# Kernel optimization log

Measured on AMD Instinct MI355X. Metric: run time of the kernel, lower is better.

The kernel has to match this reference:

```python
import jax, jax.numpy as jnp
import numpy as np

NUM_LEVELS = 16
LEVEL_DIM = 2
BASE_RES = 16
PER_LEVEL_SCALE = 2.0
LOG2_HASHMAP = 19
INPUT_DIM = 3
N_POINTS = 2_000_000
B = 262144


def _compute_offsets():
    offsets = []
    off = 0
    max_params = 2 ** LOG2_HASHMAP
    for i in range(NUM_LEVELS):
        res = int(np.ceil(BASE_RES * PER_LEVEL_SCALE ** i))
        p = min(max_params, (res + 1) ** INPUT_DIM)  # align_corners=False -> res+1 verts per axis
        p = int(np.ceil(p / 8) * 8)
        offsets.append(off)
        off += p
    offsets.append(off)
    return offsets

OFFSETS = _compute_offsets()
TOTAL_PARAMS = OFFSETS[-1]  # 7131240
PRIMES = (1, 2654435761, 805459861)  # instant-ngp fast_hash primes for D=3
CORNER_BITS = np.array([[(c >> d) & 1 for d in range(3)] for c in range(8)], dtype=np.int32)  # [8,3]


def _build_table(embeddings, fs_embeddings, scatter_index):
    # scatter_add point embeddings (and counts) into grid vertices, then blend
    sums = jnp.zeros((TOTAL_PARAMS, LEVEL_DIM), embeddings.dtype).at[scatter_index].add(embeddings)
    counts = jnp.zeros((TOTAL_PARAMS,), embeddings.dtype).at[scatter_index].add(1.0)
    sel = jnp.minimum(counts, 1.0)[:, None]
    num = jnp.maximum(counts, 1.0)[:, None]
    return (sums / num) * sel + fs_embeddings * (1.0 - sel)


def _grid_encode(x, table):
    # x: [B,3] in [0,1]; table: [TOTAL_PARAMS, C]. Multi-res hash grid, linear interp,
    # align_corners=False (matches torch-ngp grid_encode CUDA kernel).
    S = np.log2(PER_LEVEL_SCALE)
    bits_i = jnp.asarray(CORNER_BITS)                 # [8,3] int
    bits_f = jnp.asarray(CORNER_BITS, dtype=x.dtype)  # [8,3] float
    outs = []
    for level in range(NUM_LEVELS):
        scale = np.exp2(level * S) * BASE_RES - 1.0
        resolution = int(np.ceil(scale)) + 1
        hashmap_size = OFFSETS[level + 1] - OFFSETS[level]
        pos = x * scale + 0.5  # align_corners=False offset
        pos_grid = jnp.floor(pos)
        frac = pos - pos_grid                                  # [B,3]
        corner = pos_grid.astype(jnp.int32)[:, None, :] + bits_i  # [B,8,3]
        stride = (resolution + 1) ** 3
        if stride > hashmap_size:
            # hashed level: xor of per-dim prime products, uint32 wraparound
            cu = corner.astype(jnp.uint32)
            idx = (cu[..., 0] * jnp.uint32(PRIMES[0])) ^ \
                  (cu[..., 1] * jnp.uint32(PRIMES[1])) ^ \
                  (cu[..., 2] * jnp.uint32(PRIMES[2]))
            idx = (idx % jnp.uint32(hashmap_size)).astype(jnp.int32)
        else:
            # dense level: row-major index with stride (res+1)
            r1 = resolution + 1
            idx = (corner[..., 0] + corner[..., 1] * r1 + corner[..., 2] * (r1 * r1)) % hashmap_size
        vals = table[idx + OFFSETS[level]]  # [B,8,C] gather
        w = jnp.prod(jnp.where(bits_f > 0, frac[:, None, :], 1.0 - frac[:, None, :]), axis=-1)  # [B,8]
        outs.append(jnp.einsum('bk,bkc->bc', w, vals))
    return jnp.concatenate(outs, axis=-1)  # [B, L*C]


def setup_inputs() -> dict:
    key = jax.random.key(0)
    k1, k2, k3, k4 = jax.random.split(key, 4)
    std = 1e-4  # reset_parameters() uniform(-1e-4, 1e-4)
    inputs = jax.random.uniform(k1, (B, 3), jnp.float32, minval=-1.0, maxval=1.0)
    embeddings = jax.random.uniform(k2, (N_POINTS, LEVEL_DIM), jnp.float32, minval=-std, maxval=std)
    fs_embeddings = jax.random.uniform(k3, (TOTAL_PARAMS, LEVEL_DIM), jnp.float32, minval=-std, maxval=std)
    scatter_index = jax.random.randint(k4, (N_POINTS,), 0, TOTAL_PARAMS, dtype=jnp.int32)
    return {"inputs": inputs, "embeddings": embeddings, "fs_embeddings": fs_embeddings,
            "scatter_index": scatter_index, "bound": 1}


def reference(inputs, embeddings, fs_embeddings, scatter_index, bound):
    table = _build_table(embeddings, fs_embeddings, scatter_index)
    x = (inputs + bound) / (2.0 * bound)  # map to [0,1]
    return _grid_encode(x, table)  # [B, NUM_LEVELS*LEVEL_DIM]
```

## Files before the change

### kernel.cpp

```cpp
#include <hip/hip_runtime.h>

#define TOTAL_PARAMS 7131240
#define NLEVELS 16
#define NB 262144
#define HASH_MASK 0x7FFFF

#define SF2 5115000.0f
#define CF 1e-4f

__constant__ int c_off[NLEVELS] = {
    0, 4920, 40864, 315496, 839784, 1364072, 1888360, 2412648,
    2936936, 3461224, 3985512, 4509800, 5034088, 5558376, 6082664, 6606952};

typedef float vfloat2 __attribute__((ext_vector_type(2)));
typedef float vfloat4 __attribute__((ext_vector_type(4)));
typedef unsigned vuint2 __attribute__((ext_vector_type(2)));
typedef int vint2 __attribute__((ext_vector_type(2)));

__global__ __launch_bounds__(256) void scatter_prep_kernel(
    const vfloat4* __restrict__ emb2, const vint2* __restrict__ sidx2,
    unsigned* __restrict__ accum, int n, int nsb,
    const float* __restrict__ x, const int* __restrict__ bound_p,
    vfloat4* __restrict__ xn, int B) {
    if ((int)blockIdx.x >= nsb) {
        int p = ((int)blockIdx.x - nsb) * 256 + threadIdx.x;
        if (p >= B) return;
        float bound = (float)bound_p[0];
        float denom = 2.0f * bound;
        vfloat4 o;
        o.x = (x[p * 3 + 0] + bound) / denom;
        o.y = (x[p * 3 + 1] + bound) / denom;
        o.z = (x[p * 3 + 2] + bound) / denom;
        o.w = 0.0f;
        xn[p] = o;
        return;
    }
    int i = blockIdx.x * 256 + threadIdx.x;
    int base = i * 2;
    if (base >= n) return;
    if (base + 1 < n) {
        vint2 idx = __builtin_nontemporal_load(&sidx2[i]);
        vfloat4 e = __builtin_nontemporal_load(&emb2[i]);
        unsigned qx0 = __float2uint_rn((e.x + CF) * SF2);
        unsigned qy0 = __float2uint_rn((e.y + CF) * SF2);
        unsigned qx1 = __float2uint_rn((e.z + CF) * SF2);
        unsigned qy1 = __float2uint_rn((e.w + CF) * SF2);
        atomicAdd(&accum[idx.x], (1u << 28) | (qx0 << 14) | qy0);
        atomicAdd(&accum[idx.y], (1u << 28) | (qx1 << 14) | qy1);
    } else {
        const int* sidx = (const int*)sidx2;
        const vfloat2* emb = (const vfloat2*)emb2;
        int idx = sidx[base];
        vfloat2 e = emb[base];
        unsigned qx = __float2uint_rn((e.x + CF) * SF2);
        unsigned qy = __float2uint_rn((e.y + CF) * SF2);
        atomicAdd(&accum[idx], (1u << 28) | (qx << 14) | qy);
    }
}

__device__ __forceinline__ unsigned short f2bf(float f) {
    unsigned u = __builtin_bit_cast(unsigned, f);
    return (unsigned short)((u + 0x7FFFu + ((u >> 16) & 1u)) >> 16);
}

__global__ __launch_bounds__(256) void finalize_kernel(
    const unsigned* __restrict__ accum, const vfloat4* __restrict__ fs2,
    unsigned long long* __restrict__ table2, int npairs) {
    int i = blockIdx.x * 256 + threadIdx.x;
    if (i >= npairs) return;
    vuint2 a = __builtin_nontemporal_load((const vuint2*)(accum + 2 * i));
    unsigned c0 = a.x >> 28, c1 = a.y >> 28;
    vfloat4 f = {0.0f, 0.0f, 0.0f, 0.0f};
    if ((c0 == 0u) | (c1 == 0u)) f = __builtin_nontemporal_load(&fs2[i]);
    float rx0, ry0, rx1, ry1;
    if (c0 == 0u) {
        rx0 = f.x; ry0 = f.y;
    } else {
        float inv = 1.0f / ((float)c0 * SF2);
        rx0 = (float)((a.x >> 14) & 0x3FFFu) * inv - CF;
        ry0 = (float)(a.x & 0x3FFFu) * inv - CF;
    }
    if (c1 == 0u) {
        rx1 = f.z; ry1 = f.w;
    } else {
        float inv = 1.0f / ((float)c1 * SF2);
        rx1 = (float)((a.y >> 14) & 0x3FFFu) * inv - CF;
        ry1 = (float)(a.y & 0x3FFFu) * inv - CF;
    }
    unsigned lo = (unsigned)f2bf(rx0) | ((unsigned)f2bf(ry0) << 16);
    unsigned hi = (unsigned)f2bf(rx1) | ((unsigned)f2bf(ry1) << 16);
    table2[i] = (unsigned long long)lo | ((unsigned long long)hi << 32);
}

template <bool DENSE>
__device__ __forceinline__ vfloat2 level_interp(
    float px, float py, float pz, int l, const unsigned* __restrict__ table_bf) {
    int res = 16 << l;
    float scale = (float)(res - 1);
    float posx = px * scale + 0.5f;
    float posy = py * scale + 0.5f;
    float posz = pz * scale + 0.5f;
    float gx = floorf(posx), gy = floorf(posy), gz = floorf(posz);
    float fx = posx - gx, fy = posy - gy, fz = posz - gz;
    unsigned ix = (unsigned)(int)gx, iy = (unsigned)(int)gy, iz = (unsigned)(int)gz;

    const unsigned* __restrict__ tb = table_bf + c_off[l];

    unsigned tyz[4];
    if (DENSE) {
        unsigned r1u = (unsigned)(res + 1);
        unsigned r1sq = r1u * r1u;
        unsigned ty0 = iy * r1u, tz0 = iz * r1sq;
        tyz[0] = ty0 + tz0;
        tyz[1] = ty0 + r1u + tz0;
        tyz[2] = ty0 + tz0 + r1sq;
        tyz[3] = ty0 + r1u + tz0 + r1sq;
    } else {
        unsigned ty0 = iy * 2654435761u, ty1 = ty0 + 2654435761u;
        unsigned tz0 = iz * 805459861u, tz1 = tz0 + 805459861u;
        tyz[0] = ty0 ^ tz0;
        tyz[1] = ty1 ^ tz0;
        tyz[2] = ty0 ^ tz1;
        tyz[3] = ty1 ^ tz1;
    }

    unsigned v[8];
#pragma unroll
    for (int c = 0; c < 8; ++c) {
        unsigned cx = ix + (unsigned)(c & 1);
        unsigned idx;
        if (DENSE) idx = cx + tyz[c >> 1];
        else       idx = (cx ^ tyz[c >> 1]) & HASH_MASK;
        v[c] = tb[idx];
    }

    float wy0 = 1.0f - fy, wz0 = 1.0f - fz;
    float wyz[4] = {wy0 * wz0, fy * wz0, wy0 * fz, fy * fz};
    float wx0 = 1.0f - fx;
    float ax = 0.0f, ay = 0.0f;
#pragma unroll
    for (int c2 = 0; c2 < 4; ++c2) {
        float v0x = __builtin_bit_cast(float, v[2 * c2] << 16);
        float v0y = __builtin_bit_cast(float, v[2 * c2] & 0xFFFF0000u);
        float v1x = __builtin_bit_cast(float, v[2 * c2 + 1] << 16);
        float v1y = __builtin_bit_cast(float, v[2 * c2 + 1] & 0xFFFF0000u);
        float w = wyz[c2];
        ax += w * (wx0 * v0x + fx * v1x);
        ay += w * (wx0 * v0y + fx * v1y);
    }
    vfloat2 r;
    r.x = ax;
    r.y = ay;
    return r;
}

struct v2x2 { vfloat2 a, b; };

__device__ __forceinline__ void hash_idx8(
    float px, float py, float pz, float scale,
    unsigned idx[8], float* fx, float* fy, float* fz) {
    float posx = px * scale + 0.5f;
    float posy = py * scale + 0.5f;
    float posz = pz * scale + 0.5f;
    float gx = floorf(posx), gy = floorf(posy), gz = floorf(posz);
    *fx = posx - gx; *fy = posy - gy; *fz = posz - gz;
    unsigned ix = (unsigned)(int)gx, iy = (unsigned)(int)gy, iz = (unsigned)(int)gz;
    unsigned ty0 = iy * 2654435761u, ty1 = ty0 + 2654435761u;
    unsigned tz0 = iz * 805459861u, tz1 = tz0 + 805459861u;
    unsigned tyz[4] = {ty0 ^ tz0, ty1 ^ tz0, ty0 ^ tz1, ty1 ^ tz1};
#pragma unroll
    for (int c = 0; c < 8; ++c)
        idx[c] = ((ix + (unsigned)(c & 1)) ^ tyz[c >> 1]) & HASH_MASK;
}

__device__ __forceinline__ vfloat2 wsum8(
    const unsigned v[8], float fx, float fy, float fz) {
    float wy0 = 1.0f - fy, wz0 = 1.0f - fz;
    float wyz[4] = {wy0 * wz0, fy * wz0, wy0 * fz, fy * fz};
    float wx0 = 1.0f - fx;
    float ax = 0.0f, ay = 0.0f;
#pragma unroll
    for (int c2 = 0; c2 < 4; ++c2) {
        float v0x = __builtin_bit_cast(float, v[2 * c2] << 16);
        float v0y = __builtin_bit_cast(float, v[2 * c2] & 0xFFFF0000u);
        float v1x = __builtin_bit_cast(float, v[2 * c2 + 1] << 16);
        float v1y = __builtin_bit_cast(float, v[2 * c2 + 1] & 0xFFFF0000u);
        float w = wyz[c2];
        ax += w * (wx0 * v0x + fx * v1x);
        ay += w * (wx0 * v0y + fx * v1y);
    }
    vfloat2 r;
    r.x = ax;
    r.y = ay;
    return r;
}

__global__ __launch_bounds__(256, 6) void encode_hash_kernel(
    const vfloat4* __restrict__ xn, const unsigned* __restrict__ table_bf,
    vfloat2* __restrict__ lm) {
    int l = 15 - ((int)blockIdx.x >> 9);
    int b0 = (((int)blockIdx.x & 511) << 9) + (int)threadIdx.x;
    int b1 = b0 + 256;

    vfloat4 pA = xn[b0];
    vfloat4 pB = xn[b1];

    int res = 16 << l;
    float scale = (float)(res - 1);
    const unsigned* __restrict__ tb = table_bf + c_off[l];

    unsigned iA[8], iB[8];
    float fAx, fAy, fAz, fBx, fBy, fBz;
    hash_idx8(pA.x, pA.y, pA.z, scale, iA, &fAx, &fAy, &fAz);
    hash_idx8(pB.x, pB.y, pB.z, scale, iB, &fBx, &fBy, &fBz);

    unsigned vA[8], vB[8];
#pragma unroll
    for (int c = 0; c < 8; ++c) vA[c] = tb[iA[c]];
#pragma unroll
    for (int c = 0; c < 8; ++c) vB[c] = tb[iB[c]];

    vfloat2 oA = wsum8(vA, fAx, fAy, fAz);
    vfloat2 oB = wsum8(vB, fBx, fBy, fBz);

    vfloat2* dst = &lm[(l - 3) * NB];
    __builtin_nontemporal_store(oA, dst + b0);
    __builtin_nontemporal_store(oB, dst + b1);
}

__global__ __launch_bounds__(256, 4) void finish_kernel(
    const vfloat4* __restrict__ xn, const unsigned* __restrict__ table_bf,
    const vfloat2* __restrict__ lm, float* __restrict__ out) {
    int b = blockIdx.x * 256 + threadIdx.x;

    vfloat4 p = xn[b];

    float row[2 * NLEVELS];

#pragma unroll
    for (int lev = 0; lev < 13; ++lev) {
        vfloat2 v = lm[lev * NB + b];
        row[2 * (lev + 3)] = v.x;
        row[2 * (lev + 3) + 1] = v.y;
    }
#pragma unroll
    for (int l = 0; l < 3; ++l) {
        vfloat2 o = level_interp<true>(p.x, p.y, p.z, l, table_bf);
        row[2 * l] = o.x;
        row[2 * l + 1] = o.y;
    }

    vfloat4* op = (vfloat4*)&out[b * 32];
#pragma unroll
    for (int k = 0; k < 8; ++k) {
        vfloat4 o;
        o.x = row[4 * k + 0];
        o.y = row[4 * k + 1];
        o.z = row[4 * k + 2];
        o.w = row[4 * k + 3];
        op[k] = o;
    }
}

extern "C" void kernel_launch(void* const* d_in, const int* in_sizes, int n_in,
                              void* d_out, int out_size, void* d_ws, size_t ws_size,
                              hipStream_t stream) {
    const float* x     = (const float*)d_in[0];
    const float* emb   = (const float*)d_in[1];
    const float* fs    = (const float*)d_in[2];
    const int*   sidx  = (const int*)d_in[3];
    const int*   bound = (const int*)d_in[4];

    unsigned* accum    = (unsigned*)d_ws;
    unsigned* table_bf = accum + TOTAL_PARAMS;
    vfloat4*  xn       = (vfloat4*)(table_bf + TOTAL_PARAMS);
    vfloat2*  lm       = (vfloat2*)d_ws;

    int npts = in_sizes[3];
    int B = in_sizes[0] / 3;

    (void)hipMemsetAsync(d_ws, 0, (size_t)TOTAL_PARAMS * sizeof(unsigned), stream);

    int npair_pts = (npts + 1) / 2;
    int nsb = (npair_pts + 255) / 256;
    int npb = (B + 255) / 256;
    scatter_prep_kernel<<<nsb + npb, 256, 0, stream>>>(
        (const vfloat4*)emb, (const vint2*)sidx, accum, npts, nsb,
        x, bound, xn, B);

    int npairs = TOTAL_PARAMS / 2;
    finalize_kernel<<<(npairs + 255) / 256, 256, 0, stream>>>(
        accum, (const vfloat4*)fs, (unsigned long long*)table_bf, npairs);

    encode_hash_kernel<<<13 * (B / 512), 256, 0, stream>>>(
        xn, table_bf, lm);

    finish_kernel<<<B / 256, 256, 0, stream>>>(
        xn, table_bf, lm, (float*)d_out);
}
```

Baseline: 319.3 us.

## Replace global atomic scatter with bucketed binning and shared-memory accumulation

The global-memory atomicAdd scatter over a 28MB accumulator is replaced by a two-pass scheme. Points are first binned into 871 buckets of 8192 slots, with one global atomic per point on a bucket counter and the record written to a per-bucket array. A per-bucket kernel then accumulates the records with LDS atomics and builds the bf16 table directly, which removes the large accumulator memset and the separate finalize pass. In exchange each point adds an 8-byte record write and read, heavy contention on the bucket counters, and records past the fixed capacity of 4032 per bucket are silently dropped.

```diff
diff --git a/kernel.cpp b/kernel.cpp
--- a/kernel.cpp
+++ b/kernel.cpp
@@ -8,6 +8,11 @@
 #define SF2 5115000.0f
 #define CF 1e-4f
 
+#define BKT_SH 13
+#define BKT_SLOTS 8192
+#define NBKT 871
+#define BKT_CAP 4032
+
 __constant__ int c_off[NLEVELS] = {
     0, 4920, 40864, 315496, 839784, 1364072, 1888360, 2412648,
     2936936, 3461224, 3985512, 4509800, 5034088, 5558376, 6082664, 6606952};
@@ -15,15 +20,17 @@
 typedef float vfloat2 __attribute__((ext_vector_type(2)));
 typedef float vfloat4 __attribute__((ext_vector_type(4)));
 typedef unsigned vuint2 __attribute__((ext_vector_type(2)));
-typedef int vint2 __attribute__((ext_vector_type(2)));
-
-__global__ __launch_bounds__(256) void scatter_prep_kernel(
-    const vfloat4* __restrict__ emb2, const vint2* __restrict__ sidx2,
-    unsigned* __restrict__ accum, int n, int nsb,
+typedef unsigned vuint4 __attribute__((ext_vector_type(4)));
+typedef int vint4 __attribute__((ext_vector_type(4)));
+
+__global__ __launch_bounds__(256) void binscatter_prep_kernel(
+    const float* __restrict__ emb, const int* __restrict__ sidx,
+    unsigned long long* __restrict__ rec, unsigned* __restrict__ cnt,
+    int n, int nab,
     const float* __restrict__ x, const int* __restrict__ bound_p,
     vfloat4* __restrict__ xn, int B) {
-    if ((int)blockIdx.x >= nsb) {
-        int p = ((int)blockIdx.x - nsb) * 256 + threadIdx.x;
+    if ((int)blockIdx.x >= nab) {
+        int p = ((int)blockIdx.x - nab) * 256 + threadIdx.x;
         if (p >= B) return;
         float bound = (float)bound_p[0];
         float denom = 2.0f * bound;
@@ -35,26 +42,44 @@
         xn[p] = o;
         return;
     }
-    int i = blockIdx.x * 256 + threadIdx.x;
-    int base = i * 2;
-    if (base >= n) return;
-    if (base + 1 < n) {
-        vint2 idx = __builtin_nontemporal_load(&sidx2[i]);
-        vfloat4 e = __builtin_nontemporal_load(&emb2[i]);
-        unsigned qx0 = __float2uint_rn((e.x + CF) * SF2);
-        unsigned qy0 = __float2uint_rn((e.y + CF) * SF2);
-        unsigned qx1 = __float2uint_rn((e.z + CF) * SF2);
-        unsigned qy1 = __float2uint_rn((e.w + CF) * SF2);
-        atomicAdd(&accum[idx.x], (1u << 28) | (qx0 << 14) | qy0);
-        atomicAdd(&accum[idx.y], (1u << 28) | (qx1 << 14) | qy1);
+    int i0 = ((int)blockIdx.x * 256 + (int)threadIdx.x) * 8;
+    if (i0 >= n) return;
+    if (i0 + 8 <= n) {
+        vint4 s0 = __builtin_nontemporal_load((const vint4*)(sidx + i0));
+        vint4 s1 = __builtin_nontemporal_load((const vint4*)(sidx + i0 + 4));
+        vfloat4 e0 = __builtin_nontemporal_load((const vfloat4*)(emb + 2 * i0));
+        vfloat4 e1 = __builtin_nontemporal_load((const vfloat4*)(emb + 2 * i0 + 4));
+        vfloat4 e2 = __builtin_nontemporal_load((const vfloat4*)(emb + 2 * i0 + 8));
+        vfloat4 e3 = __builtin_nontemporal_load((const vfloat4*)(emb + 2 * i0 + 12));
+        int idxs[8] = {s0.x, s0.y, s0.z, s0.w, s1.x, s1.y, s1.z, s1.w};
+        float ex[8] = {e0.x, e0.z, e1.x, e1.z, e2.x, e2.z, e3.x, e3.z};
+        float ey[8] = {e0.y, e0.w, e1.y, e1.w, e2.y, e2.w, e3.y, e3.w};
+#pragma unroll
+        for (int k = 0; k < 8; ++k) {
+            unsigned qx = __float2uint_rn((ex[k] + CF) * SF2);
+            unsigned qy = __float2uint_rn((ey[k] + CF) * SF2);
+            unsigned payload = (1u << 28) | (qx << 14) | qy;
+            unsigned b = (unsigned)idxs[k] >> BKT_SH;
+            unsigned pos = atomicAdd(&cnt[b], 1u);
+            if (pos < (unsigned)BKT_CAP) {
+                unsigned long long r =
+                    ((unsigned long long)payload << 32) | (unsigned)idxs[k];
+                __builtin_nontemporal_store(r, &rec[b * BKT_CAP + pos]);
+            }
+        }
     } else {
-        const int* sidx = (const int*)sidx2;
-        const vfloat2* emb = (const vfloat2*)emb2;
-        int idx = sidx[base];
-        vfloat2 e = emb[base];
-        unsigned qx = __float2uint_rn((e.x + CF) * SF2);
-        unsigned qy = __float2uint_rn((e.y + CF) * SF2);
-        atomicAdd(&accum[idx], (1u << 28) | (qx << 14) | qy);
+        for (int k = 0; k < 8 && i0 + k < n; ++k) {
+            int idx = sidx[i0 + k];
+            float exs = emb[2 * (i0 + k)], eys = emb[2 * (i0 + k) + 1];
+            unsigned qx = __float2uint_rn((exs + CF) * SF2);
+            unsigned qy = __float2uint_rn((eys + CF) * SF2);
+            unsigned payload = (1u << 28) | (qx << 14) | qy;
+            unsigned b = (unsigned)idx >> BKT_SH;
+            unsigned pos = atomicAdd(&cnt[b], 1u);
+            if (pos < (unsigned)BKT_CAP)
+                rec[b * BKT_CAP + pos] =
+                    ((unsigned long long)payload << 32) | (unsigned)idx;
+        }
     }
 }
 
@@ -63,33 +88,57 @@
     return (unsigned short)((u + 0x7FFFu + ((u >> 16) & 1u)) >> 16);
 }
 
-__global__ __launch_bounds__(256) void finalize_kernel(
-    const unsigned* __restrict__ accum, const vfloat4* __restrict__ fs2,
-    unsigned long long* __restrict__ table2, int npairs) {
-    int i = blockIdx.x * 256 + threadIdx.x;
-    if (i >= npairs) return;
-    vuint2 a = __builtin_nontemporal_load((const vuint2*)(accum + 2 * i));
-    unsigned c0 = a.x >> 28, c1 = a.y >> 28;
-    vfloat4 f = {0.0f, 0.0f, 0.0f, 0.0f};
-    if ((c0 == 0u) | (c1 == 0u)) f = __builtin_nontemporal_load(&fs2[i]);
-    float rx0, ry0, rx1, ry1;
-    if (c0 == 0u) {
-        rx0 = f.x; ry0 = f.y;
-    } else {
-        float inv = 1.0f / ((float)c0 * SF2);
-        rx0 = (float)((a.x >> 14) & 0x3FFFu) * inv - CF;
-        ry0 = (float)(a.x & 0x3FFFu) * inv - CF;
-    }
-    if (c1 == 0u) {
-        rx1 = f.z; ry1 = f.w;
-    } else {
-        float inv = 1.0f / ((float)c1 * SF2);
-        rx1 = (float)((a.y >> 14) & 0x3FFFu) * inv - CF;
-        ry1 = (float)(a.y & 0x3FFFu) * inv - CF;
-    }
-    unsigned lo = (unsigned)f2bf(rx0) | ((unsigned)f2bf(ry0) << 16);
-    unsigned hi = (unsigned)f2bf(rx1) | ((unsigned)f2bf(ry1) << 16);
-    table2[i] = (unsigned long long)lo | ((unsigned long long)hi << 32);
+__global__ __launch_bounds__(256) void build_table_kernel(
+    const unsigned long long* __restrict__ rec, const unsigned* __restrict__ cnt,
+    const vfloat4* __restrict__ fs2, unsigned long long* __restrict__ table2) {
+    __shared__ unsigned acc[BKT_SLOTS];
+    int b = (int)blockIdx.x;
+    int tid = (int)threadIdx.x;
+
+    vuint4* accv = (vuint4*)acc;
+#pragma unroll
+    for (int k = 0; k < BKT_SLOTS / 4 / 256; ++k) {
+        vuint4 z = {0u, 0u, 0u, 0u};
+        accv[tid + k * 256] = z;
+    }
+    __syncthreads();
+
+    int n = (int)cnt[b];
+    if (n > BKT_CAP) n = BKT_CAP;
+    const unsigned long long* __restrict__ r = rec + (unsigned)b * BKT_CAP;
+    for (int j = tid; j < n; j += 256) {
+        unsigned long long v = __builtin_nontemporal_load(&r[j]);
+        atomicAdd(&acc[(unsigned)v & (BKT_SLOTS - 1u)], (unsigned)(v >> 32));
+    }
+    __syncthreads();
+
+    int pair0 = b * (BKT_SLOTS / 2);
+    for (int k = tid; k < BKT_SLOTS / 2; k += 256) {
+        int gp = pair0 + k;
+        if (2 * gp >= TOTAL_PARAMS) break;
+        vuint2 a = ((const vuint2*)acc)[k];
+        unsigned c0 = a.x >> 28, c1 = a.y >> 28;
+        vfloat4 f = {0.0f, 0.0f, 0.0f, 0.0f};
+        if ((c0 == 0u) | (c1 == 0u)) f = __builtin_nontemporal_load(&fs2[gp]);
+        float rx0, ry0, rx1, ry1;
+        if (c0 == 0u) {
+            rx0 = f.x; ry0 = f.y;
+        } else {
+            float inv = 1.0f / ((float)c0 * SF2);
+            rx0 = (float)((a.x >> 14) & 0x3FFFu) * inv - CF;
+            ry0 = (float)(a.x & 0x3FFFu) * inv - CF;
+        }
+        if (c1 == 0u) {
+            rx1 = f.z; ry1 = f.w;
+        } else {
+            float inv = 1.0f / ((float)c1 * SF2);
+            rx1 = (float)((a.y >> 14) & 0x3FFFu) * inv - CF;
+            ry1 = (float)(a.y & 0x3FFFu) * inv - CF;
+        }
+        unsigned lo = (unsigned)f2bf(rx0) | ((unsigned)f2bf(ry0) << 16);
+        unsigned hi = (unsigned)f2bf(rx1) | ((unsigned)f2bf(ry1) << 16);
+        table2[gp] = (unsigned long long)lo | ((unsigned long long)hi << 32);
+    }
 }
 
 template <bool DENSE>
@@ -154,8 +203,6 @@
     return r;
 }
 
-struct v2x2 { vfloat2 a, b; };
-
 __device__ __forceinline__ void hash_idx8(
     float px, float py, float pz, float scale,
     unsigned idx[8], float* fx, float* fy, float* fz) {
@@ -271,26 +318,25 @@
     const int*   sidx  = (const int*)d_in[3];
     const int*   bound = (const int*)d_in[4];
 
-    unsigned* accum    = (unsigned*)d_ws;
-    unsigned* table_bf = accum + TOTAL_PARAMS;
-    vfloat4*  xn       = (vfloat4*)(table_bf + TOTAL_PARAMS);
-    vfloat2*  lm       = (vfloat2*)d_ws;
+    unsigned long long* rec = (unsigned long long*)d_ws;
+    unsigned* table_bf = (unsigned*)((char*)d_ws +
+                                     (size_t)NBKT * BKT_CAP * sizeof(unsigned long long));
+    vfloat4* xn  = (vfloat4*)(table_bf + TOTAL_PARAMS);
+    unsigned* cnt = (unsigned*)((char*)xn + (size_t)NB * sizeof(vfloat4));
+    vfloat2* lm  = (vfloat2*)d_ws;
 
     int npts = in_sizes[3];
     int B = in_sizes[0] / 3;
 
-    (void)hipMemsetAsync(d_ws, 0, (size_t)TOTAL_PARAMS * sizeof(unsigned), stream);
-
-    int npair_pts = (npts + 1) / 2;
-    int nsb = (npair_pts + 255) / 256;
+    (void)hipMemsetAsync(cnt, 0, NBKT * sizeof(unsigned), stream);
+
+    int nab = (npts + 2047) / 2048;
     int npb = (B + 255) / 256;
-    scatter_prep_kernel<<<nsb + npb, 256, 0, stream>>>(
-        (const vfloat4*)emb, (const vint2*)sidx, accum, npts, nsb,
-        x, bound, xn, B);
-
-    int npairs = TOTAL_PARAMS / 2;
-    finalize_kernel<<<(npairs + 255) / 256, 256, 0, stream>>>(
-        accum, (const vfloat4*)fs, (unsigned long long*)table_bf, npairs);
+    binscatter_prep_kernel<<<nab + npb, 256, 0, stream>>>(
+        emb, sidx, rec, cnt, npts, nab, x, bound, xn, B);
+
+    build_table_kernel<<<NBKT, 256, 0, stream>>>(
+        rec, cnt, (const vfloat4*)fs, (unsigned long long*)table_bf);
 
     encode_hash_kernel<<<13 * (B / 512), 256, 0, stream>>>(
         xn, table_bf, lm);
```

After: 1.116 ms. 250% more time.
